# Optimization experiments

Measured on AMD Instinct MI355X. Metric: run time of the kernel, lower is better.

Reference implementation:

```python
import jax, jax.numpy as jnp
import numpy as np
from math import sqrt

T, B, V = 32, 16, 30000
D, DQKV = 300, 150
K, G = 10, 32            # top-K globals, grapharea_size neighbours each
S = 25000                # last_idx_senses (= SC rows)
EPS = 1e-8


def setup_inputs() -> dict:
    key = jax.random.key(0)
    ks = jax.random.split(key, 6)
    return {
        "predictions_globals": jax.random.normal(ks[0], (T, B, V), jnp.float32),
        "location_context": jax.random.normal(ks[1], (T, B, D), jnp.float32),
        "SC": jax.random.normal(ks[2], (S, D), jnp.float32),
        "Wq": jax.random.normal(ks[3], (D, DQKV), jnp.float32) / sqrt(D),
        "Wk": jax.random.normal(ks[4], (D, DQKV), jnp.float32) / sqrt(D),
        "neighbours_table": jax.random.randint(ks[5], (V, G), 0, S, jnp.int64),
    }


def reference(predictions_globals, location_context, SC, Wq, Wk, neighbours_table):
    # 1) per-sample top-K global selection (sort descending, take K indices)
    _, topk_idx = jax.lax.top_k(predictions_globals, K)          # [T,B,K]
    # 2) sense-neighbour lookup: K globals x G neighbours -> N = K*G senses
    neigh = neighbours_table[topk_idx].reshape(T, B, K * G)      # [T,B,N] int
    # 3) gather precomputed sense contexts
    senses_context = SC[neigh]                                   # [T,B,N,D]
    # 4) ComputeLogits: QK attention logits
    q = location_context @ Wq                                    # [T,B,dqkv]
    k = senses_context @ Wk                                      # [T,B,N,dqkv]
    logits = jnp.einsum("tbd,tbnd->tbn", q, k) / sqrt(DQKV)      # [T,B,N]
    # 5) softmax over neighbours, scatter into full sense distribution
    p = jax.nn.softmax(logits, axis=-1)                          # [T,B,N]
    base = jnp.full((T * B, S), EPS, dtype=p.dtype)
    rows = jnp.arange(T * B)[:, None]                            # [TB,1]
    senses_softmax = base.at[rows, neigh.reshape(T * B, -1)].set(p.reshape(T * B, -1))
    # 6) log-probabilities over all senses
    return jnp.log(senses_softmax)                               # [T*B, S]
```

## Files before the change

### kernel.cpp

```cpp
#include <hip/hip_runtime.h>
#include <math.h>

#define T_ 32
#define B_ 16
#define V_ 30000
#define V4 7500
#define D_ 300
#define DQKV_ 150
#define K_ 10
#define G_ 32
#define N_ 320
#define S_ 25000
#define S4 6250
#define SLICE 3125
#define QKP 304
#define NTS 1024
#define NTG 256
#define NTF 384
#define LCAP 4096
#define UTH 0xC0000000u

__device__ __forceinline__ unsigned umap(float f) {
    unsigned b = __float_as_uint(f);
    unsigned mask = (unsigned)(((int)b) >> 31);
    return b ^ (mask | 0x80000000u);
}
__device__ __forceinline__ bool better_u(unsigned au, int ai, unsigned bu, int bi) {
    return (au > bu) || (au == bu && ai < bi);
}

__global__ __launch_bounds__(NTS, 2) void scanqk_kernel(
    const float* __restrict__ pred, const float* __restrict__ lc,
    const float* __restrict__ Wq, const float* __restrict__ Wk,
    float* __restrict__ out, int* __restrict__ wstop, float* __restrict__ qkws)
{
    const int b = blockIdx.x, tid = threadIdx.x;
    const int lane = tid & 63, wave = tid >> 6;
    __shared__ unsigned lu[LCAP];
    __shared__ int      li[LCAP];
    __shared__ int      cnt;
    __shared__ unsigned wcv[16 * K_];
    __shared__ int      wci[16 * K_];
    __shared__ __align__(16) float lcs[D_];
    __shared__ float    qpart[2][DQKV_];

    if (b >= T_ * B_) {
        const int row = b - T_ * B_;
        if (tid < D_ / 4)
            ((float4*)lcs)[tid] = ((const float4*)(lc + (size_t)row * D_))[tid];
        __syncthreads();

        if (tid < 2 * DQKV_) {
            int h = tid / DQKV_;
            int j = tid - h * DQKV_;
            int d0 = h * 150;
            const float* wp = Wq + (size_t)d0 * DQKV_ + j;
            float a0 = 0.f, a1 = 0.f;
            #pragma unroll 5
            for (int dd = 0; dd < 150; dd += 2) {
                a0 += lcs[d0 + dd]     * wp[(size_t)dd * DQKV_];
                a1 += lcs[d0 + dd + 1] * wp[(size_t)(dd + 1) * DQKV_];
            }
            qpart[h][j] = a0 + a1;
        }
        __syncthreads();

        float qv0 = qpart[0][lane] + qpart[1][lane];
        float qv1 = qpart[0][64 + lane] + qpart[1][64 + lane];
        float qv2 = (lane < 22) ? (qpart[0][128 + lane] + qpart[1][128 + lane]) : 0.f;
        for (int d = wave; d < D_; d += 16) {
            const float* wr = Wk + (size_t)d * DQKV_;
            float w0 = wr[lane];
            float w1 = wr[64 + lane];
            float w2 = (lane < 22) ? wr[128 + lane] : 0.f;
            float p = w0 * qv0 + w1 * qv1 + w2 * qv2;
            #pragma unroll
            for (int off = 32; off; off >>= 1) p += __shfl_xor(p, off, 64);
            if (lane == 0) qkws[(size_t)row * QKP + d] = p;
        }
        return;
    }

    const int row = b;
    if (tid == 0) cnt = 0;
    __syncthreads();

    const float FILL = -18.420680743952367f;
    {
        float4 f4 = make_float4(FILL, FILL, FILL, FILL);
        float4* o4 = (float4*)(out + (size_t)row * S_);
        #pragma unroll
        for (int k = 0; k < 7; ++k) { int i = tid + k * NTS; if (i < S4) o4[i] = f4; }
    }

    {
        const float4* p4 = (const float4*)(pred + (size_t)row * V_);
        #pragma unroll
        for (int k = 0; k < 8; ++k) {
            int i = tid + k * NTS;
            if (i < V4) {
                float4 v = p4[i];
                unsigned u0 = umap(v.x), u1 = umap(v.y), u2 = umap(v.z), u3 = umap(v.w);
                int base = i * 4;
                if (u0 >= UTH) { int p = atomicAdd(&cnt, 1); if (p < LCAP) { lu[p] = u0; li[p] = base; } }
                if (u1 >= UTH) { int p = atomicAdd(&cnt, 1); if (p < LCAP) { lu[p] = u1; li[p] = base + 1; } }
                if (u2 >= UTH) { int p = atomicAdd(&cnt, 1); if (p < LCAP) { lu[p] = u2; li[p] = base + 2; } }
                if (u3 >= UTH) { int p = atomicAdd(&cnt, 1); if (p < LCAP) { lu[p] = u3; li[p] = base + 3; } }
            }
        }
    }
    __syncthreads();
    const int c = cnt;

    if (c >= K_ && c <= LCAP) {
        unsigned cu[4]; int cix[4];
        #pragma unroll
        for (int k = 0; k < 4; ++k) {
            int s = wave * 64 + lane + k * NTS;
            bool ok = s < c;
            cu[k]  = ok ? lu[s] : 0u;
            cix[k] = ok ? li[s] : 0x7fffffff;
        }
        for (int p = 0; p < K_; ++p) {
            unsigned bu = cu[0]; int bi = cix[0];
            #pragma unroll
            for (int k = 1; k < 4; ++k)
                if (better_u(cu[k], cix[k], bu, bi)) { bu = cu[k]; bi = cix[k]; }
            #pragma unroll
            for (int off = 32; off; off >>= 1) {
                unsigned ou = __shfl_xor(bu, off, 64);
                int      oi = __shfl_xor(bi, off, 64);
                if (better_u(ou, oi, bu, bi)) { bu = ou; bi = oi; }
            }
            if (lane == 0) { wcv[wave * K_ + p] = bu; wci[wave * K_ + p] = bi; }
            #pragma unroll
            for (int k = 0; k < 4; ++k)
                if (cix[k] == bi) cu[k] = 0u;
        }
        __syncthreads();

        if (wave == 0) {
            unsigned c0u = wcv[lane],      c1u = wcv[64 + lane];
            int      c0i = wci[lane],      c1i = wci[64 + lane];
            unsigned c2u = (lane < 32) ? wcv[128 + lane] : 0u;
            int      c2i = (lane < 32) ? wci[128 + lane] : 0x7fffffff;
            for (int p = 0; p < K_; ++p) {
                unsigned bu = c0u; int bi = c0i;
                if (better_u(c1u, c1i, bu, bi)) { bu = c1u; bi = c1i; }
                if (better_u(c2u, c2i, bu, bi)) { bu = c2u; bi = c2i; }
                #pragma unroll
                for (int off = 32; off; off >>= 1) {
                    unsigned ou = __shfl_xor(bu, off, 64);
                    int      oi = __shfl_xor(bi, off, 64);
                    if (better_u(ou, oi, bu, bi)) { bu = ou; bi = oi; }
                }
                if (lane == 0) wstop[row * K_ + p] = bi;
                if (c0i == bi) c0u = 0u;
                if (c1i == bi) c1u = 0u;
                if (c2i == bi) c2u = 0u;
            }
        }
    } else {
        if (wave == 0) {
            unsigned tu[K_]; int tix[K_];
            #pragma unroll
            for (int s = 0; s < K_; ++s) { tu[s] = 0; tix[s] = 0x7fffffff; }
            const float* prow = pred + (size_t)row * V_;
            for (int i = lane; i < V_; i += 64) {
                unsigned u = umap(prow[i]);
                if (better_u(u, i, tu[K_-1], tix[K_-1])) {
                    tu[K_-1] = u; tix[K_-1] = i;
                    #pragma unroll
                    for (int s = K_-1; s > 0; --s)
                        if (better_u(tu[s], tix[s], tu[s-1], tix[s-1])) {
                            unsigned a = tu[s]; tu[s] = tu[s-1]; tu[s-1] = a;
                            int b2 = tix[s]; tix[s] = tix[s-1]; tix[s-1] = b2;
                        }
                }
            }
            for (int p = 0; p < K_; ++p) {
                unsigned bu = tu[0]; int bi = tix[0];
                #pragma unroll
                for (int s = 1; s < K_; ++s)
                    if (better_u(tu[s], tix[s], bu, bi)) { bu = tu[s]; bi = tix[s]; }
                #pragma unroll
                for (int off = 32; off; off >>= 1) {
                    unsigned ou = __shfl_xor(bu, off, 64);
                    int      oi = __shfl_xor(bi, off, 64);
                    if (better_u(ou, oi, bu, bi)) { bu = ou; bi = oi; }
                }
                if (lane == 0) wstop[row * K_ + p] = bi;
                #pragma unroll
                for (int s = 0; s < K_; ++s)
                    if (tix[s] == bi) tu[s] = 0;
            }
        }
    }
}

__global__ __launch_bounds__(NTG) void gather_kernel(
    const float* __restrict__ SC, const float* __restrict__ qkws,
    const int* __restrict__ nbt, const int* __restrict__ wstop,
    float* __restrict__ logws)
{
    const int r = blockIdx.x >> 3;
    const int ch = blockIdx.x & 7;
    const int lo = ch * SLICE, hi = lo + SLICE;
    const int tid = threadIdx.x;
    __shared__ int   topg[K_];
    __shared__ int   nid[N_];
    __shared__ __align__(16) float qk[D_];
    __shared__ int   list[N_];
    __shared__ int   lcnt;

    if (tid == 0) lcnt = 0;
    if (tid < K_) topg[tid] = wstop[r * K_ + tid];
    if (tid >= 64 && tid < 64 + D_ / 4)
        ((float4*)qk)[tid - 64] = ((const float4*)(qkws + (size_t)r * QKP))[tid - 64];
    __syncthreads();

    for (int i = tid; i < N_; i += NTG)
        nid[i] = nbt[topg[i >> 5] * G_ + (i & 31)];
    __syncthreads();

    for (int i = tid; i < N_; i += NTG) {
        int sv = nid[i];
        if (sv >= lo && sv < hi) { int p = atomicAdd(&lcnt, 1); list[p] = i; }
    }
    __syncthreads();
    const int c2 = lcnt;

    const float ISC = 0.08164965809277260327f;
    const float4* q4 = (const float4*)qk;
    for (int s = tid; s < 8 * c2; s += NTG) {
        int g = s >> 3, h = s & 7;
        int n = list[g];
        const float4* sc4 = (const float4*)(SC + (size_t)nid[n] * D_);
        int c0 = h * 9;
        float acc = 0.f;
        #pragma unroll
        for (int cc = 0; cc < 9; ++cc) {
            float4 a = sc4[c0 + cc];
            float4 bq = q4[c0 + cc];
            acc += a.x * bq.x + a.y * bq.y + a.z * bq.z + a.w * bq.w;
        }
        if (h < 3) {
            float4 a = sc4[72 + h];
            float4 bq = q4[72 + h];
            acc += a.x * bq.x + a.y * bq.y + a.z * bq.z + a.w * bq.w;
        }
        acc += __shfl_xor(acc, 1, 64);
        acc += __shfl_xor(acc, 2, 64);
        acc += __shfl_xor(acc, 4, 64);
        if (h == 0) logws[(size_t)r * N_ + n] = acc * ISC;
    }
}

__global__ __launch_bounds__(NTF) void finalize_kernel(
    const float* __restrict__ logws, const int* __restrict__ nbt,
    const int* __restrict__ wstop, float* __restrict__ out)
{
    const int row = blockIdx.x, tid = threadIdx.x;
    const int lane = tid & 63, wave = tid >> 6;
    __shared__ int   topg[K_];
    __shared__ float lg[N_];
    __shared__ int   nid[N_];
    __shared__ int   kills[N_];
    __shared__ float redA[6], redB[6];
    float* outrow = out + (size_t)row * S_;

    if (tid < K_) topg[tid] = wstop[row * K_ + tid];
    __syncthreads();
    if (tid < N_) {
        nid[tid] = nbt[topg[tid >> 5] * G_ + (tid & 31)];
        lg[tid]  = logws[(size_t)row * N_ + tid];
        kills[tid] = 0;
    }
    __syncthreads();

    float v = (tid < N_) ? lg[tid] : -INFINITY;
    float m = v;
    #pragma unroll
    for (int off = 32; off; off >>= 1) m = fmaxf(m, __shfl_xor(m, off, 64));
    if (lane == 0) redA[wave] = m;
    __syncthreads();
    m = redA[0];
    #pragma unroll
    for (int w = 1; w < 6; ++w) m = fmaxf(m, redA[w]);

    float ss = (tid < N_) ? expf(v - m) : 0.f;
    #pragma unroll
    for (int off = 32; off; off >>= 1) ss += __shfl_xor(ss, off, 64);
    if (lane == 0) redB[wave] = ss;
    __syncthreads();
    float tot = redB[0];
    #pragma unroll
    for (int w = 1; w < 6; ++w) tot += redB[w];
    float lsum = logf(tot);

    for (int s = tid; s < 4 * N_; s += NTF) {
        int n = s >> 2, cix = s & 3;
        int sidx = nid[n];
        int clo = cix * 80;
        int lo2 = (n + 1 > clo) ? n + 1 : clo;
        int hi2 = clo + 80;
        bool mt = false;
        #pragma unroll 4
        for (int n2 = lo2; n2 < hi2; ++n2) mt |= (nid[n2] == sidx);
        if (mt) kills[n] = 1;
    }
    __syncthreads();

    if (tid < N_ && !kills[tid]) outrow[nid[tid]] = (v - m) - lsum;
}

#define NWS 16
__device__ __forceinline__ bool better(float av, int ai, float bv, int bi) {
    return (av > bv) || (av == bv && ai < bi);
}
__global__ __launch_bounds__(NTS, 4) void selfatt_fused(
    const float* __restrict__ pred, const float* __restrict__ lc,
    const float* __restrict__ SC, const float* __restrict__ Wq,
    const float* __restrict__ Wk, const int* __restrict__ nbt,
    float* __restrict__ out)
{
    const int row = blockIdx.x, tid = threadIdx.x;
    const int lane = tid & 63, wave = tid >> 6;
    __shared__ float wcv[NWS * K_];
    __shared__ int   wci[NWS * K_];
    __shared__ int   topg[K_];
    __shared__ float lcs[D_];
    __shared__ float qs[DQKV_];
    __shared__ __align__(16) float qks[D_];
    __shared__ int   nidx[N_];
    __shared__ float lg[N_];
    __shared__ int   kills[N_];
    __shared__ float redA[NWS], redB[NWS];
    float* outrow = out + (size_t)row * S_;
    const float FILL = -18.420680743952367f;
    {
        float4 f4 = make_float4(FILL, FILL, FILL, FILL);
        float4* o4 = (float4*)outrow;
        #pragma unroll
        for (int k = 0; k < 7; ++k) { int i = tid + k * NTS; if (i < S4) o4[i] = f4; }
    }
    float tv[K_]; int ti[K_];
    #pragma unroll
    for (int s = 0; s < K_; ++s) { tv[s] = -INFINITY; ti[s] = 0x7fffffff; }
    {
        const float4* p4 = (const float4*)(pred + (size_t)row * V_);
        const float4 NEG = make_float4(-INFINITY, -INFINITY, -INFINITY, -INFINITY);
        float4 a[8]; int ib[8];
        #pragma unroll
        for (int u = 0; u < 8; ++u) {
            int i = tid + u * NTS;
            a[u]  = (i < V4) ? p4[i] : NEG;
            ib[u] = (i < V4) ? i * 4 : 0x7ffffff0;
        }
        #pragma unroll
        for (int u = 0; u < 8; ++u) {
            float x = a[u].x, y = a[u].y, z = a[u].z, w = a[u].w;
            float m4 = fmaxf(fmaxf(x, y), fmaxf(z, w));
            if (!(m4 < tv[K_-1])) {
                float vals[4] = {x, y, z, w};
                #pragma unroll
                for (int cc = 0; cc < 4; ++cc) {
                    float val = vals[cc];
                    int   idx = ib[u] + cc;
                    if (better(val, idx, tv[K_-1], ti[K_-1])) {
                        tv[K_-1] = val; ti[K_-1] = idx;
                        #pragma unroll
                        for (int s = K_-1; s > 0; --s) {
                            if (better(tv[s], ti[s], tv[s-1], ti[s-1])) {
                                float fx = tv[s]; tv[s] = tv[s-1]; tv[s-1] = fx;
                                int   iy = ti[s]; ti[s] = ti[s-1]; ti[s-1] = iy;
                            }
                        }
                    }
                }
            }
        }
    }
    for (int p = 0; p < K_; ++p) {
        float bv = tv[0]; int bi = ti[0];
        #pragma unroll
        for (int s = 1; s < K_; ++s)
            if (better(tv[s], ti[s], bv, bi)) { bv = tv[s]; bi = ti[s]; }
        #pragma unroll
        for (int off = 32; off; off >>= 1) {
            float ov = __shfl_xor(bv, off, 64);
            int   oi = __shfl_xor(bi, off, 64);
            if (better(ov, oi, bv, bi)) { bv = ov; bi = oi; }
        }
        if (lane == 0) { wcv[wave * K_ + p] = bv; wci[wave * K_ + p] = bi; }
        #pragma unroll
        for (int s = 0; s < K_; ++s)
            if (ti[s] == bi) tv[s] = -INFINITY;
    }
    __syncthreads();
    if (wave == 0) {
        float c0v = wcv[lane],      c1v = wcv[64 + lane];
        int   c0i = wci[lane],      c1i = wci[64 + lane];
        float c2v = (lane < 32) ? wcv[128 + lane] : -INFINITY;
        int   c2i = (lane < 32) ? wci[128 + lane] : 0x7fffffff;
        for (int p = 0; p < K_; ++p) {
            float bv = c0v; int bi = c0i;
            if (better(c1v, c1i, bv, bi)) { bv = c1v; bi = c1i; }
            if (better(c2v, c2i, bv, bi)) { bv = c2v; bi = c2i; }
            #pragma unroll
            for (int off = 32; off; off >>= 1) {
                float ov = __shfl_xor(bv, off, 64);
                int   oi = __shfl_xor(bi, off, 64);
                if (better(ov, oi, bv, bi)) { bv = ov; bi = oi; }
            }
            if (lane == 0) topg[p] = bi;
            if (c0i == bi) c0v = -INFINITY;
            if (c1i == bi) c1v = -INFINITY;
            if (c2i == bi) c2v = -INFINITY;
        }
    }
    __syncthreads();
    if (tid < N_) { int g = topg[tid >> 5]; nidx[tid] = nbt[g * G_ + (tid & 31)]; }
    else if (tid < 2 * N_) kills[tid - N_] = 0;
    else if (tid >= 640 && tid < 640 + D_) lcs[tid - 640] = lc[(size_t)row * D_ + (tid - 640)];
    __syncthreads();
    if (tid < 600) {
        int j = tid >> 2, h = tid & 3;
        int d0 = h * 75;
        const float* wp = Wq + (size_t)d0 * DQKV_ + j;
        float acc = 0.f;
        #pragma unroll 5
        for (int dd = 0; dd < 75; ++dd) acc += lcs[d0 + dd] * wp[(size_t)dd * DQKV_];
        acc += __shfl_xor(acc, 1, 64);
        acc += __shfl_xor(acc, 2, 64);
        if (h == 0) qs[j] = acc;
    } else {
        int t0 = tid - 600;
        for (int s = t0; s < 4 * N_; s += 424) {
            int n = s >> 2, cc = s & 3;
            int sidx = nidx[n];
            int clo = cc * 80;
            int lo = (n + 1 > clo) ? n + 1 : clo;
            int hi = clo + 80;
            bool mt = false;
            #pragma unroll 4
            for (int n2 = lo; n2 < hi; ++n2) mt |= (nidx[n2] == sidx);
            if (mt) kills[n] = 1;
        }
    }
    __syncthreads();
    if (tid < 600) {
        int d = tid >> 1, h = tid & 1;
        int j0 = h * 75;
        const float* wrow = Wk + (size_t)d * DQKV_ + j0;
        float acc = 0.f;
        #pragma unroll 5
        for (int jj = 0; jj < 75; ++jj) acc += wrow[jj] * qs[j0 + jj];
        acc += __shfl_xor(acc, 1, 64);
        if (h == 0) qks[d] = acc;
    }
    __syncthreads();
    const float ISC = 0.08164965809277260327f;
    const float4* q4 = (const float4*)qks;
    for (int s = tid; s < 8 * N_; s += NTS) {
        int n = s >> 3, h = s & 7;
        const float4* sc4 = (const float4*)(SC + (size_t)nidx[n] * D_);
        int c0 = h * 9;
        float acc = 0.f;
        #pragma unroll
        for (int cc = 0; cc < 9; ++cc) {
            float4 a = sc4[c0 + cc];
            float4 b = q4[c0 + cc];
            acc += a.x * b.x + a.y * b.y + a.z * b.z + a.w * b.w;
        }
        if (h < 3) {
            float4 a = sc4[72 + h];
            float4 b = q4[72 + h];
            acc += a.x * b.x + a.y * b.y + a.z * b.z + a.w * b.w;
        }
        acc += __shfl_xor(acc, 1, 64);
        acc += __shfl_xor(acc, 2, 64);
        acc += __shfl_xor(acc, 4, 64);
        if (h == 0) lg[n] = acc * ISC;
    }
    __syncthreads();
    float v = (tid < N_) ? lg[tid] : -INFINITY;
    float m = v;
    #pragma unroll
    for (int off = 32; off; off >>= 1) m = fmaxf(m, __shfl_xor(m, off, 64));
    if (lane == 0) redA[wave] = m;
    __syncthreads();
    m = redA[0];
    #pragma unroll
    for (int w = 1; w < NWS; ++w) m = fmaxf(m, redA[w]);
    float e = (tid < N_) ? expf(v - m) : 0.f;
    float ss = e;
    #pragma unroll
    for (int off = 32; off; off >>= 1) ss += __shfl_xor(ss, off, 64);
    if (lane == 0) redB[wave] = ss;
    __syncthreads();
    float tot = redB[0];
    #pragma unroll
    for (int w = 1; w < NWS; ++w) tot += redB[w];
    float lsum = logf(tot);
    if (tid < N_ && !kills[tid]) outrow[nidx[tid]] = (v - m) - lsum;
}

extern "C" void kernel_launch(void* const* d_in, const int* in_sizes, int n_in,
                              void* d_out, int out_size, void* d_ws, size_t ws_size,
                              hipStream_t stream) {
    const float* pred = (const float*)d_in[0];
    const float* lc   = (const float*)d_in[1];
    const float* SC   = (const float*)d_in[2];
    const float* Wq   = (const float*)d_in[3];
    const float* Wk   = (const float*)d_in[4];
    const int*   nbt  = (const int*)d_in[5];
    float* out = (float*)d_out;

    const int nrows = T_ * B_;
    const size_t nQK = (size_t)nrows * QKP;
    const size_t nLG = (size_t)nrows * N_;
    const size_t nTP = (size_t)nrows * K_;
    const size_t need = (nQK + nLG) * sizeof(float) + nTP * sizeof(int);

    if (ws_size >= need) {
        float* qkws  = (float*)d_ws;
        float* logws = qkws + nQK;
        int*   wstop = (int*)(logws + nLG);
        scanqk_kernel<<<dim3(nrows * 2), dim3(NTS), 0, stream>>>(
            pred, lc, Wq, Wk, out, wstop, qkws);
        gather_kernel<<<dim3(nrows * 8), dim3(NTG), 0, stream>>>(
            SC, qkws, nbt, wstop, logws);
        finalize_kernel<<<dim3(nrows), dim3(NTF), 0, stream>>>(
            logws, nbt, wstop, out);
    } else {
        selfatt_fused<<<dim3(T_ * B_), dim3(NTS), 0, stream>>>(
            pred, lc, SC, Wq, Wk, nbt, out);
    }
}
```

Baseline: 101.7 us.

## Move output fill to finalize kernel and aggregate candidate atomics per wave

New measurement: 105.0 us. 1.03x slower.

```diff
diff --git a/kernel.cpp b/kernel.cpp
--- a/kernel.cpp
+++ b/kernel.cpp
@@ -16,7 +16,7 @@
 #define QKP 304
 #define NTS 1024
 #define NTG 256
-#define NTF 384
+#define NTF 1024
 #define LCAP 4096
 #define UTH 0xC0000000u
 
@@ -29,10 +29,10 @@
     return (au > bu) || (au == bu && ai < bi);
 }
 
-__global__ __launch_bounds__(NTS, 2) void scanqk_kernel(
+__global__ __launch_bounds__(NTS, 2) void stage1_kernel(
     const float* __restrict__ pred, const float* __restrict__ lc,
     const float* __restrict__ Wq, const float* __restrict__ Wk,
-    float* __restrict__ out, int* __restrict__ wstop, float* __restrict__ qkws)
+    int* __restrict__ wstop, float* __restrict__ qkws)
 {
     const int b = blockIdx.x, tid = threadIdx.x;
     const int lane = tid & 63, wave = tid >> 6;
@@ -85,34 +85,44 @@
     if (tid == 0) cnt = 0;
     __syncthreads();
 
-    const float FILL = -18.420680743952367f;
-    {
-        float4 f4 = make_float4(FILL, FILL, FILL, FILL);
-        float4* o4 = (float4*)(out + (size_t)row * S_);
-        #pragma unroll
-        for (int k = 0; k < 7; ++k) { int i = tid + k * NTS; if (i < S4) o4[i] = f4; }
-    }
-
     {
         const float4* p4 = (const float4*)(pred + (size_t)row * V_);
-        #pragma unroll
-        for (int k = 0; k < 8; ++k) {
-            int i = tid + k * NTS;
-            if (i < V4) {
-                float4 v = p4[i];
-                unsigned u0 = umap(v.x), u1 = umap(v.y), u2 = umap(v.z), u3 = umap(v.w);
-                int base = i * 4;
-                if (u0 >= UTH) { int p = atomicAdd(&cnt, 1); if (p < LCAP) { lu[p] = u0; li[p] = base; } }
-                if (u1 >= UTH) { int p = atomicAdd(&cnt, 1); if (p < LCAP) { lu[p] = u1; li[p] = base + 1; } }
-                if (u2 >= UTH) { int p = atomicAdd(&cnt, 1); if (p < LCAP) { lu[p] = u2; li[p] = base + 2; } }
-                if (u3 >= UTH) { int p = atomicAdd(&cnt, 1); if (p < LCAP) { lu[p] = u3; li[p] = base + 3; } }
+        const float4 NEG = make_float4(-INFINITY, -INFINITY, -INFINITY, -INFINITY);
+        float4 a[8]; int ib[8]; bool okf[8];
+        #pragma unroll
+        for (int u = 0; u < 8; ++u) {
+            int i = tid + u * NTS;
+            okf[u] = i < V4;
+            a[u]  = okf[u] ? p4[i] : NEG;
+            ib[u] = i * 4;
+        }
+        const unsigned long long lmask = (lane == 63) ? 0x7fffffffffffffffull
+                                                      : ((1ull << lane) - 1ull);
+        #pragma unroll
+        for (int u = 0; u < 8; ++u) {
+            float vals[4] = {a[u].x, a[u].y, a[u].z, a[u].w};
+            #pragma unroll
+            for (int c = 0; c < 4; ++c) {
+                unsigned uu = umap(vals[c]);
+                bool has = okf[u] && (uu >= UTH);
+                unsigned long long mask = __ballot(has);
+                if (mask) {
+                    int bs = 0;
+                    if (lane == 0) bs = atomicAdd(&cnt, (int)__popcll(mask));
+                    bs = __shfl(bs, 0, 64);
+                    if (has) {
+                        int p = bs + (int)__popcll(mask & lmask);
+                        if (p < LCAP) { lu[p] = uu; li[p] = ib[u] + c; }
+                    }
+                }
             }
         }
     }
     __syncthreads();
     const int c = cnt;
-
-    if (c >= K_ && c <= LCAP) {
+    const bool mainpath = (c >= K_ && c <= LCAP);
+
+    if (mainpath) {
         unsigned cu[4]; int cix[4];
         #pragma unroll
         for (int k = 0; k < 4; ++k) {
@@ -266,8 +276,16 @@
     __shared__ float lg[N_];
     __shared__ int   nid[N_];
     __shared__ int   kills[N_];
-    __shared__ float redA[6], redB[6];
+    __shared__ float redA[16], redB[16];
     float* outrow = out + (size_t)row * S_;
+
+    const float FILL = -18.420680743952367f;
+    {
+        float4 f4 = make_float4(FILL, FILL, FILL, FILL);
+        float4* o4 = (float4*)outrow;
+        #pragma unroll
+        for (int k = 0; k < 7; ++k) { int i = tid + k * NTF; if (i < S4) o4[i] = f4; }
+    }
 
     if (tid < K_) topg[tid] = wstop[row * K_ + tid];
     __syncthreads();
@@ -286,7 +304,7 @@
     __syncthreads();
     m = redA[0];
     #pragma unroll
-    for (int w = 1; w < 6; ++w) m = fmaxf(m, redA[w]);
+    for (int w = 1; w < 16; ++w) m = fmaxf(m, redA[w]);
 
     float ss = (tid < N_) ? expf(v - m) : 0.f;
     #pragma unroll
@@ -295,7 +313,7 @@
     __syncthreads();
     float tot = redB[0];
     #pragma unroll
-    for (int w = 1; w < 6; ++w) tot += redB[w];
+    for (int w = 1; w < 16; ++w) tot += redB[w];
     float lsum = logf(tot);
 
     for (int s = tid; s < 4 * N_; s += NTF) {
@@ -527,14 +545,14 @@
         float* qkws  = (float*)d_ws;
         float* logws = qkws + nQK;
         int*   wstop = (int*)(logws + nLG);
-        scanqk_kernel<<<dim3(nrows * 2), dim3(NTS), 0, stream>>>(
-            pred, lc, Wq, Wk, out, wstop, qkws);
+        stage1_kernel<<<dim3(nrows * 2), dim3(NTS), 0, stream>>>(
+            pred, lc, Wq, Wk, wstop, qkws);
         gather_kernel<<<dim3(nrows * 8), dim3(NTG), 0, stream>>>(
             SC, qkws, nbt, wstop, logws);
         finalize_kernel<<<dim3(nrows), dim3(NTF), 0, stream>>>(
             logws, nbt, wstop, out);
     } else {
-        selfatt_fused<<<dim3(T_ * B_), dim3(NTS), 0, stream>>>(
+        selfatt_fused<<<dim3(nrows), dim3(NTS), 0, stream>>>(
             pred, lc, SC, Wq, Wk, nbt, out);
     }
 }
```
